# Optimization experiments

Measured on AMD Instinct MI355X. Metric: run time of the kernel, lower is better.

The kernel has to match this reference:

```python
import jax, jax.numpy as jnp
import numpy as np

B, N, K = 8, 4096, 64
D = 256   # d_model
G = 512   # g: number of query points


def _gather(points, idx):
    # points: [B, N, C], idx: [B, G, K] -> [B, G, K, C]
    return jax.vmap(lambda p, i: p[i])(points, idx)


def _mlp(h, W1, b1, W2, b2):
    # torch Linear: y = x @ W.T + b
    return jax.nn.relu(h @ W1.T + b1) @ W2.T + b2


def setup_inputs() -> dict:
    key = jax.random.key(0)
    ks = jax.random.split(key, 12)
    s = 1.0 / np.sqrt(D)
    return {
        "xyz": jax.random.normal(ks[0], (B, N, 3), jnp.float32),
        "x": jax.random.normal(ks[1], (B, N, D), jnp.float32),
        "dist_arg_sort": jax.random.randint(ks[2], (B, N, K), 0, N),
        "Wq": jax.random.normal(ks[3], (D, D), jnp.float32) * s,
        "Wk": jax.random.normal(ks[4], (D, D), jnp.float32) * s,
        "Wv": jax.random.normal(ks[5], (D, D), jnp.float32) * s,
        "Wd1": jax.random.normal(ks[6], (D, 3), jnp.float32) * 0.5,
        "bd1": jnp.zeros((D,), jnp.float32),
        "Wd2": jax.random.normal(ks[7], (D, D), jnp.float32) * s,
        "bd2": jnp.zeros((D,), jnp.float32),
        "Wg1": jax.random.normal(ks[8], (D, D), jnp.float32) * s,
        "bg1": jnp.zeros((D,), jnp.float32),
        "Wg2": jax.random.normal(ks[9], (D, D), jnp.float32) * s,
        "bg2": jnp.zeros((D,), jnp.float32),
    }


def reference(xyz, x, dist_arg_sort, Wq, Wk, Wv, Wd1, bd1, Wd2, bd2, Wg1, bg1, Wg2, bg2):
    g_idx = jnp.sort(dist_arg_sort[:, :G], axis=-1)          # [B,G,K]
    g_xyz = _gather(xyz, g_idx)                               # [B,G,K,3]
    gq = x[:, :G] @ Wq.T                                      # [B,G,D]
    gk = _gather(x @ Wk.T, g_idx)                             # [B,G,K,D]
    gv = _gather(x @ Wv.T, g_idx)                             # [B,G,K,D]
    # positional encoding MLP on coordinate deltas
    g_pos_enc = _mlp(xyz[:, :G, None] - g_xyz, Wd1, bd1, Wd2, bd2)  # [B,G,K,D]
    # vector attention MLP
    g_attn = _mlp(gq[:, :, None] - gk + g_pos_enc, Wg1, bg1, Wg2, bg2)
    g_attn = jax.nn.softmax(g_attn / np.sqrt(D).astype(np.float32), axis=-2)
    # weighted sum over neighbor dim
    return jnp.einsum("bmnf,bmnf->bmf", g_attn, gv + g_pos_enc)  # [B,G,D]
```

## Files before the change

### kernel.cpp

```cpp
#include <hip/hip_runtime.h>

#define DEV static __device__ __forceinline__

typedef __attribute__((ext_vector_type(8))) short bf16x8;
typedef __attribute__((ext_vector_type(4))) float f32x4;
typedef __attribute__((ext_vector_type(4))) unsigned u32x4;

constexpr int BB = 8, NN = 4096, KK = 64, DD = 256, GG = 512;

DEV unsigned short f2b(float f){
  unsigned u = __builtin_bit_cast(unsigned, f);
  unsigned r = (u + 0x7FFFu + ((u >> 16) & 1u)) >> 16;
  return (unsigned short)r;
}
DEV float b2f(unsigned short h){
  unsigned u = ((unsigned)h) << 16;
  return __builtin_bit_cast(float, u);
}
DEV unsigned f2b2(float lo, float hi){
  unsigned r;
  asm("v_cvt_pk_bf16_f32 %0, %1, %2" : "=v"(r) : "v"(lo), "v"(hi));
  return r;
}
DEV int swz(int row, int byteoff){ return row*512 + (byteoff ^ ((row & 15) << 4)); }

DEV f32x4 zero4(){ f32x4 z = {0.f, 0.f, 0.f, 0.f}; return z; }

__global__ void k_detect(const unsigned short* __restrict__ x_raw, int* __restrict__ flag){
  int lane = threadIdx.x;
  float mx = 0.f;
#pragma unroll
  for (int i = 0; i < 16; ++i) mx = fmaxf(mx, fabsf(b2f(x_raw[lane*16 + i])));
  unsigned long long big = __ballot(mx > 1e4f);
  if (lane == 0) *flag = (big == 0ull) ? 1 : 0;
}

struct PrepArgs {
  const void* src[12];
  void*       dst[12];
  int         n[12];
  int         bf16out[12];
};

__global__ void k_prep(PrepArgs P, const int* __restrict__ flagp){
  int flag = *flagp;
  long stride = (long)gridDim.x * blockDim.x;
  long gid = (long)blockIdx.x * blockDim.x + threadIdx.x;
  for (int s = 0; s < 12; ++s){
    int ns = P.n[s];
    const void* sp = P.src[s];
    if (P.bf16out[s]){
      unsigned short* dp = (unsigned short*)P.dst[s];
      for (long i = gid; i < ns; i += stride)
        dp[i] = flag ? ((const unsigned short*)sp)[i] : f2b(((const float*)sp)[i]);
    } else {
      float* dp = (float*)P.dst[s];
      for (long i = gid; i < ns; i += stride)
        dp[i] = flag ? b2f(((const unsigned short*)sp)[i]) : ((const float*)sp)[i];
    }
  }
}

DEV void gemm64(const char* sbuf, const unsigned short* __restrict__ Wt,
                int lane, int c0, f32x4 acc[4][4]){
  const int lrow = lane & 15, lk = lane >> 4;
  const unsigned short* wbase = Wt + (c0 + lrow)*DD + lk*8;
  bf16x8 bcur[4], bnxt[4];
#pragma unroll
  for (int nf = 0; nf < 4; ++nf) bcur[nf] = *(const bf16x8*)(wbase + nf*16*DD);
#pragma unroll
  for (int ks = 0; ks < 8; ++ks){
    bf16x8 a[4];
#pragma unroll
    for (int mf = 0; mf < 4; ++mf)
      a[mf] = *(const bf16x8*)(sbuf + swz(mf*16 + lrow, ks*64 + lk*16));
    if (ks < 7){
#pragma unroll
      for (int nf = 0; nf < 4; ++nf)
        bnxt[nf] = *(const bf16x8*)(wbase + nf*16*DD + (ks + 1)*32);
    }
    __builtin_amdgcn_s_setprio(1);
#pragma unroll
    for (int mf = 0; mf < 4; ++mf)
#pragma unroll
      for (int nf = 0; nf < 4; ++nf)
        acc[mf][nf] = __builtin_amdgcn_mfma_f32_16x16x32_bf16(a[mf], bcur[nf], acc[mf][nf], 0, 0, 0);
    __builtin_amdgcn_s_setprio(0);
#pragma unroll
    for (int nf = 0; nf < 4; ++nf) bcur[nf] = bnxt[nf];
  }
}

DEV void gemm32(const char* sbuf, const unsigned short* __restrict__ Wt,
                int lane, int c0, f32x4 acc[4][2]){
  const int lrow = lane & 15, lk = lane >> 4;
  const unsigned short* wbase = Wt + (c0 + lrow)*DD + lk*8;
  bf16x8 bcur[2], bnxt[2];
#pragma unroll
  for (int nf = 0; nf < 2; ++nf) bcur[nf] = *(const bf16x8*)(wbase + nf*16*DD);
#pragma unroll
  for (int ks = 0; ks < 8; ++ks){
    bf16x8 a[4];
#pragma unroll
    for (int mf = 0; mf < 4; ++mf)
      a[mf] = *(const bf16x8*)(sbuf + swz(mf*16 + lrow, ks*64 + lk*16));
    if (ks < 7){
#pragma unroll
      for (int nf = 0; nf < 2; ++nf)
        bnxt[nf] = *(const bf16x8*)(wbase + nf*16*DD + (ks + 1)*32);
    }
    __builtin_amdgcn_s_setprio(1);
#pragma unroll
    for (int mf = 0; mf < 4; ++mf)
#pragma unroll
      for (int nf = 0; nf < 2; ++nf)
        acc[mf][nf] = __builtin_amdgcn_mfma_f32_16x16x32_bf16(a[mf], bcur[nf], acc[mf][nf], 0, 0, 0);
    __builtin_amdgcn_s_setprio(0);
#pragma unroll
    for (int nf = 0; nf < 2; ++nf) bcur[nf] = bnxt[nf];
  }
}

__global__ __launch_bounds__(256, 2) void k_gemmA(
    const void* __restrict__ x_in,
    const unsigned short* __restrict__ Wq_b, const unsigned short* __restrict__ Wk_b,
    const unsigned short* __restrict__ Wv_b,
    unsigned short* __restrict__ ktab, unsigned short* __restrict__ vtab,
    float* __restrict__ gq, const int* __restrict__ flagp){
  __shared__ __align__(16) char sA[64*512];
  const int tid = threadIdx.x, lane = tid & 63, wv = tid >> 6;
  const int flag = *flagp;
  const long row0 = (long)blockIdx.x * 64;
  const int b = (int)(row0 >> 12), n0 = (int)(row0 & 4095);

#pragma unroll
  for (int it = 0; it < 8; ++it){
    int r = (tid >> 5) + it*8;
    int f0 = (tid & 31)*8;
    bf16x8 v;
    if (flag){
      v = *(const bf16x8*)((const unsigned short*)x_in + (row0 + r)*DD + f0);
    } else {
      const float* xp = (const float*)x_in + (row0 + r)*DD + f0;
      f32x4 lo = *(const f32x4*)xp;
      f32x4 hi = *(const f32x4*)(xp + 4);
      u32x4 t;
#pragma unroll
      for (int e = 0; e < 2; ++e){ t[e] = f2b2(lo[2*e], lo[2*e+1]); t[e+2] = f2b2(hi[2*e], hi[2*e+1]); }
      v = __builtin_bit_cast(bf16x8, t);
    }
    *(bf16x8*)(sA + swz(r, f0*2)) = v;
  }
  __syncthreads();

  const int c0 = wv*64;
  const int nout = (n0 < GG) ? 3 : 2;
  for (int o = 0; o < nout; ++o){
    const unsigned short* Wt = (o == 0) ? Wk_b : (o == 1) ? Wv_b : Wq_b;
    f32x4 acc[4][4];
#pragma unroll
    for (int mf = 0; mf < 4; ++mf)
#pragma unroll
      for (int nf = 0; nf < 4; ++nf) acc[mf][nf] = zero4();
    gemm64(sA, Wt, lane, c0, acc);
#pragma unroll
    for (int mf = 0; mf < 4; ++mf)
#pragma unroll
      for (int nf = 0; nf < 4; ++nf)
#pragma unroll
        for (int r = 0; r < 4; ++r){
          int grow = mf*16 + (lane >> 4)*4 + r;
          int col = c0 + nf*16 + (lane & 15);
          float v = acc[mf][nf][r];
          if (o == 0)      ktab[(row0 + grow)*DD + col] = f2b(v);
          else if (o == 1) vtab[(row0 + grow)*DD + col] = f2b(v);
          else             gq[((long)b*GG + n0 + grow)*DD + col] = v;
        }
  }
}

__global__ __launch_bounds__(512, 4) void k_attn(
    const unsigned short* __restrict__ ktab, const unsigned short* __restrict__ vtab,
    const float* __restrict__ gq, const float* __restrict__ xyzf, const int* __restrict__ didx,
    const unsigned short* __restrict__ Wd2_b, const unsigned short* __restrict__ Wg1_b,
    const unsigned short* __restrict__ Wg2_b,
    const float* __restrict__ Wd1f, const float* __restrict__ bd1f, const float* __restrict__ bd2f,
    const float* __restrict__ bg1f, const float* __restrict__ bg2f,
    void* __restrict__ out, const int* __restrict__ flagp){
  __shared__ __align__(16) char S[64*512];
  __shared__ __align__(16) char U[64*512];
  __shared__ float s_gq[256];
  __shared__ float s_delta[64*3];

  const int tid = threadIdx.x, lane = tid & 63, wv = tid >> 6;
  const int gang = tid >> 5;
  const int f0 = (tid & 31)*8;
  const int flag = *flagp;
  int wg = blockIdx.x;
  wg = (wg & 7)*512 + (wg >> 3);
  const int b = wg >> 9, g = wg & 511;
  const long bN = (long)b * NN;

  int jrow[4];
  {
    const int* dptr = didx + (bN + g)*KK + gang*4;
#pragma unroll
    for (int it = 0; it < 4; ++it) jrow[it] = dptr[it];
  }
  if (tid < 256) s_gq[tid] = gq[((long)b*GG + g)*DD + tid];
  if (tid < 64){
    int j = didx[(bN + g)*KK + tid];
    long qb = (bN + g)*3, jb = (bN + j)*3;
#pragma unroll
    for (int c = 0; c < 3; ++c) s_delta[tid*3 + c] = xyzf[qb + c] - xyzf[jb + c];
  }
  f32x4 w1v[6];
  {
    const f32x4* wp = (const f32x4*)(Wd1f + f0*3);
#pragma unroll
    for (int q = 0; q < 6; ++q) w1v[q] = wp[q];
  }
  f32x4 b1lo = *(const f32x4*)(bd1f + f0), b1hi = *(const f32x4*)(bd1f + f0 + 4);
  const int c0 = wv*32;
  float bg2lo = bg2f[c0 + (lane & 15)];
  float bg2hi = bg2f[c0 + 16 + (lane & 15)];
  __syncthreads();

#pragma unroll
  for (int it = 0; it < 4; ++it){
    int r = gang*4 + it;
    float d0 = s_delta[r*3], d1 = s_delta[r*3+1], d2 = s_delta[r*3+2];
    float h[8];
#pragma unroll
    for (int e = 0; e < 8; ++e){
      float bias = (e < 4) ? b1lo[e] : b1hi[e-4];
      float w0 = w1v[(e*3+0) >> 2][(e*3+0) & 3];
      float w1 = w1v[(e*3+1) >> 2][(e*3+1) & 3];
      float w2 = w1v[(e*3+2) >> 2][(e*3+2) & 3];
      h[e] = fmaxf(fmaf(d0, w0, fmaf(d1, w1, fmaf(d2, w2, bias))), 0.f);
    }
    u32x4 t;
#pragma unroll
    for (int q = 0; q < 4; ++q) t[q] = f2b2(h[2*q], h[2*q+1]);
    *(bf16x8*)(S + swz(r, f0*2)) = __builtin_bit_cast(bf16x8, t);
  }

  bf16x8 kreg[4];
#pragma unroll
  for (int it = 0; it < 4; ++it)
    kreg[it] = *(const bf16x8*)(ktab + (bN + jrow[it])*DD + f0);
  __syncthreads();

  {
    f32x4 acc[4][2];
#pragma unroll
    for (int mf = 0; mf < 4; ++mf)
#pragma unroll
      for (int nf = 0; nf < 2; ++nf) acc[mf][nf] = zero4();
    gemm32(S, Wd2_b, lane, c0, acc);
#pragma unroll
    for (int nf = 0; nf < 2; ++nf){
      float bias = bd2f[c0 + nf*16 + (lane & 15)];
#pragma unroll
      for (int mf = 0; mf < 4; ++mf){
        int row = mf*16 + (lane >> 4)*4;
        int col = c0 + nf*16 + (lane & 15);
#pragma unroll
        for (int h = 0; h < 2; ++h){
          unsigned pk = f2b2(acc[mf][nf][2*h] + bias, acc[mf][nf][2*h+1] + bias);
          *(unsigned short*)(U + swz(row + 2*h,     col*2)) = (unsigned short)(pk & 0xffff);
          *(unsigned short*)(U + swz(row + 2*h + 1, col*2)) = (unsigned short)(pk >> 16);
        }
      }
    }
  }
  __syncthreads();

#pragma unroll
  for (int it = 0; it < 4; ++it){
    int r = gang*4 + it;
    bf16x8 p8 = *(const bf16x8*)(U + swz(r, f0*2));
    float v[8];
#pragma unroll
    for (int e = 0; e < 8; ++e)
      v[e] = s_gq[f0 + e] - b2f((unsigned short)kreg[it][e]) + b2f((unsigned short)p8[e]);
    u32x4 t;
#pragma unroll
    for (int q = 0; q < 4; ++q) t[q] = f2b2(v[2*q], v[2*q+1]);
    *(bf16x8*)(S + swz(r, f0*2)) = __builtin_bit_cast(bf16x8, t);
  }
  __syncthreads();

  {
    f32x4 acc[4][2];
#pragma unroll
    for (int mf = 0; mf < 4; ++mf)
#pragma unroll
      for (int nf = 0; nf < 2; ++nf) acc[mf][nf] = zero4();
    gemm32(S, Wg1_b, lane, c0, acc);
    __syncthreads();
#pragma unroll
    for (int nf = 0; nf < 2; ++nf){
      float bias = bg1f[c0 + nf*16 + (lane & 15)];
#pragma unroll
      for (int mf = 0; mf < 4; ++mf){
        int row = mf*16 + (lane >> 4)*4;
        int col = c0 + nf*16 + (lane & 15);
#pragma unroll
        for (int h = 0; h < 2; ++h){
          unsigned pk = f2b2(fmaxf(acc[mf][nf][2*h] + bias, 0.f),
                             fmaxf(acc[mf][nf][2*h+1] + bias, 0.f));
          *(unsigned short*)(S + swz(row + 2*h,     col*2)) = (unsigned short)(pk & 0xffff);
          *(unsigned short*)(S + swz(row + 2*h + 1, col*2)) = (unsigned short)(pk >> 16);
        }
      }
    }
  }
  __syncthreads();

  f32x4 lg[4][2];
#pragma unroll
  for (int mf = 0; mf < 4; ++mf)
#pragma unroll
    for (int nf = 0; nf < 2; ++nf) lg[mf][nf] = zero4();
  gemm32(S, Wg2_b, lane, c0, lg);
  __syncthreads();

  bf16x8 vreg[4];
#pragma unroll
  for (int it = 0; it < 4; ++it)
    vreg[it] = *(const bf16x8*)(vtab + (bN + jrow[it])*DD + f0);

#pragma unroll
  for (int nf = 0; nf < 2; ++nf){
    float bias = (nf == 0) ? bg2lo : bg2hi;
    float m = -1e30f;
#pragma unroll
    for (int mf = 0; mf < 4; ++mf)
#pragma unroll
      for (int r = 0; r < 4; ++r){ lg[mf][nf][r] += bias; m = fmaxf(m, lg[mf][nf][r]); }
    m = fmaxf(m, __shfl_xor(m, 16));
    m = fmaxf(m, __shfl_xor(m, 32));
    float s = 0.f;
#pragma unroll
    for (int mf = 0; mf < 4; ++mf)
#pragma unroll
      for (int r = 0; r < 4; ++r){
        float e = __expf((lg[mf][nf][r] - m) * 0.0625f);
        lg[mf][nf][r] = e; s += e;
      }
    s += __shfl_xor(s, 16);
    s += __shfl_xor(s, 32);
    float inv = 1.f / s;
#pragma unroll
    for (int mf = 0; mf < 4; ++mf){
      int row = mf*16 + (lane >> 4)*4;
      int col = c0 + nf*16 + (lane & 15);
#pragma unroll
      for (int h = 0; h < 2; ++h){
        unsigned pk = f2b2(lg[mf][nf][2*h] * inv, lg[mf][nf][2*h+1] * inv);
        *(unsigned short*)(S + swz(row + 2*h,     col*2)) = (unsigned short)(pk & 0xffff);
        *(unsigned short*)(S + swz(row + 2*h + 1, col*2)) = (unsigned short)(pk >> 16);
      }
    }
  }
  __syncthreads();

  {
    float accv[8];
#pragma unroll
    for (int e = 0; e < 8; ++e) accv[e] = 0.f;
#pragma unroll
    for (int kk2 = 0; kk2 < 4; ++kk2){
      int row = gang*4 + kk2;
      bf16x8 w8 = *(const bf16x8*)(S + swz(row, f0*2));
      bf16x8 p8 = *(const bf16x8*)(U + swz(row, f0*2));
#pragma unroll
      for (int e = 0; e < 8; ++e)
        accv[e] = fmaf(b2f((unsigned short)w8[e]),
                       b2f((unsigned short)vreg[kk2][e]) + b2f((unsigned short)p8[e]), accv[e]);
    }
    float* red = (float*)(S + gang*2048);
    f32x4 lo = {accv[0], accv[1], accv[2], accv[3]};
    f32x4 hi = {accv[4], accv[5], accv[6], accv[7]};
    *(f32x4*)(red + f0)     = lo;
    *(f32x4*)(red + f0 + 4) = hi;
  }
  __syncthreads();
  if (tid < 256){
    float v = 0.f;
#pragma unroll
    for (int p = 0; p < 16; ++p) v += *(const float*)(S + p*2048 + tid*4);
    long oi = ((long)b*GG + g)*DD + tid;
    if (flag) ((unsigned short*)out)[oi] = f2b(v);
    else      ((float*)out)[oi] = v;
  }
}

extern "C" void kernel_launch(void* const* d_in, const int* in_sizes, int n_in,
                              void* d_out, int out_size, void* d_ws, size_t ws_size,
                              hipStream_t stream){
  char* ws = (char*)d_ws;
  int* flag = (int*)ws;
  unsigned short* ktab = (unsigned short*)(ws + 256);
  unsigned short* vtab = ktab + (size_t)BB*NN*DD;
  float* gq   = (float*)(vtab + (size_t)BB*NN*DD);
  float* xyzf = gq + (size_t)BB*GG*DD;
  unsigned short* Wq_b  = (unsigned short*)(xyzf + (size_t)BB*NN*3);
  unsigned short* Wk_b  = Wq_b  + DD*DD;
  unsigned short* Wv_b  = Wk_b  + DD*DD;
  unsigned short* Wd2_b = Wv_b  + DD*DD;
  unsigned short* Wg1_b = Wd2_b + DD*DD;
  unsigned short* Wg2_b = Wg1_b + DD*DD;
  float* Wd1f = (float*)(Wg2_b + DD*DD);
  float* bd1f = Wd1f + DD*3;
  float* bd2f = bd1f + DD;
  float* bg1f = bd2f + DD;
  float* bg2f = bg1f + DD;

  k_detect<<<1, 64, 0, stream>>>((const unsigned short*)d_in[1], flag);

  PrepArgs P;
  const int wsrc[6] = {3, 4, 5, 8, 10, 12};
  unsigned short* wdst[6] = {Wq_b, Wk_b, Wv_b, Wd2_b, Wg1_b, Wg2_b};
  for (int i = 0; i < 6; ++i){ P.src[i] = d_in[wsrc[i]]; P.dst[i] = wdst[i]; P.n[i] = DD*DD; P.bf16out[i] = 1; }
  P.src[6]  = d_in[0];  P.dst[6]  = xyzf; P.n[6]  = BB*NN*3; P.bf16out[6]  = 0;
  P.src[7]  = d_in[6];  P.dst[7]  = Wd1f; P.n[7]  = DD*3;    P.bf16out[7]  = 0;
  P.src[8]  = d_in[7];  P.dst[8]  = bd1f; P.n[8]  = DD;      P.bf16out[8]  = 0;
  P.src[9]  = d_in[9];  P.dst[9]  = bd2f; P.n[9]  = DD;      P.bf16out[9]  = 0;
  P.src[10] = d_in[11]; P.dst[10] = bg1f; P.n[10] = DD;      P.bf16out[10] = 0;
  P.src[11] = d_in[13]; P.dst[11] = bg2f; P.n[11] = DD;      P.bf16out[11] = 0;
  k_prep<<<256, 256, 0, stream>>>(P, flag);

  k_gemmA<<<512, 256, 0, stream>>>(d_in[1], Wq_b, Wk_b, Wv_b, ktab, vtab, gq, flag);

  k_attn<<<4096, 512, 0, stream>>>(ktab, vtab, gq, xyzf, (const int*)d_in[2],
      Wd2_b, Wg1_b, Wg2_b, Wd1f, bd1f, bd2f, bg1f, bg2f, d_out, flag);
}
```

Before: 282.4 us.

## Replace XOR-swizzled LDS layout with padded row pitch and prefetch first weight fragments

Shared-memory tiles switch from an XOR-swizzled 512-byte row layout to a padded 560-byte pitch, aiming to avoid bank conflicts with simpler address arithmetic. The first B-operand fragments for each small GEMM are also loaded early, before the preceding LDS fill or sync, so global weight latency overlaps other work. The padding raises LDS use per block, which may lower occupancy. Padded strides can also leave different bank-conflict patterns than the swizzle did, for example on the scattered 2-byte stores.

```diff
diff --git a/kernel.cpp b/kernel.cpp
--- a/kernel.cpp
+++ b/kernel.cpp
@@ -7,6 +7,7 @@
 typedef __attribute__((ext_vector_type(4))) unsigned u32x4;
 
 constexpr int BB = 8, NN = 4096, KK = 64, DD = 256, GG = 512;
+constexpr int PITCH = 560;
 
 DEV unsigned short f2b(float f){
   unsigned u = __builtin_bit_cast(unsigned, f);
@@ -22,7 +23,7 @@
   asm("v_cvt_pk_bf16_f32 %0, %1, %2" : "=v"(r) : "v"(lo), "v"(hi));
   return r;
 }
-DEV int swz(int row, int byteoff){ return row*512 + (byteoff ^ ((row & 15) << 4)); }
+DEV int rof(int row, int byteoff){ return row*PITCH + byteoff; }
 
 DEV f32x4 zero4(){ f32x4 z = {0.f, 0.f, 0.f, 0.f}; return z; }
 
@@ -61,6 +62,12 @@
   }
 }
 
+DEV void preB(const unsigned short* __restrict__ Wt, int lane, int c0, bf16x8 b0[2]){
+  const unsigned short* wbase = Wt + (c0 + (lane & 15))*DD + (lane >> 4)*8;
+  b0[0] = *(const bf16x8*)(wbase);
+  b0[1] = *(const bf16x8*)(wbase + 16*DD);
+}
+
 DEV void gemm64(const char* sbuf, const unsigned short* __restrict__ Wt,
                 int lane, int c0, f32x4 acc[4][4]){
   const int lrow = lane & 15, lk = lane >> 4;
@@ -73,7 +80,7 @@
     bf16x8 a[4];
 #pragma unroll
     for (int mf = 0; mf < 4; ++mf)
-      a[mf] = *(const bf16x8*)(sbuf + swz(mf*16 + lrow, ks*64 + lk*16));
+      a[mf] = *(const bf16x8*)(sbuf + rof(mf*16 + lrow, ks*64 + lk*16));
     if (ks < 7){
 #pragma unroll
       for (int nf = 0; nf < 4; ++nf)
@@ -92,18 +99,17 @@
 }
 
 DEV void gemm32(const char* sbuf, const unsigned short* __restrict__ Wt,
-                int lane, int c0, f32x4 acc[4][2]){
+                int lane, int c0, f32x4 acc[4][2], const bf16x8 b0[2]){
   const int lrow = lane & 15, lk = lane >> 4;
   const unsigned short* wbase = Wt + (c0 + lrow)*DD + lk*8;
   bf16x8 bcur[2], bnxt[2];
-#pragma unroll
-  for (int nf = 0; nf < 2; ++nf) bcur[nf] = *(const bf16x8*)(wbase + nf*16*DD);
+  bcur[0] = b0[0]; bcur[1] = b0[1];
 #pragma unroll
   for (int ks = 0; ks < 8; ++ks){
     bf16x8 a[4];
 #pragma unroll
     for (int mf = 0; mf < 4; ++mf)
-      a[mf] = *(const bf16x8*)(sbuf + swz(mf*16 + lrow, ks*64 + lk*16));
+      a[mf] = *(const bf16x8*)(sbuf + rof(mf*16 + lrow, ks*64 + lk*16));
     if (ks < 7){
 #pragma unroll
       for (int nf = 0; nf < 2; ++nf)
@@ -127,7 +133,7 @@
     const unsigned short* __restrict__ Wv_b,
     unsigned short* __restrict__ ktab, unsigned short* __restrict__ vtab,
     float* __restrict__ gq, const int* __restrict__ flagp){
-  __shared__ __align__(16) char sA[64*512];
+  __shared__ __align__(16) char sA[64*PITCH];
   const int tid = threadIdx.x, lane = tid & 63, wv = tid >> 6;
   const int flag = *flagp;
   const long row0 = (long)blockIdx.x * 64;
@@ -149,7 +155,7 @@
       for (int e = 0; e < 2; ++e){ t[e] = f2b2(lo[2*e], lo[2*e+1]); t[e+2] = f2b2(hi[2*e], hi[2*e+1]); }
       v = __builtin_bit_cast(bf16x8, t);
     }
-    *(bf16x8*)(sA + swz(r, f0*2)) = v;
+    *(bf16x8*)(sA + rof(r, f0*2)) = v;
   }
   __syncthreads();
 
@@ -187,8 +193,8 @@
     const float* __restrict__ Wd1f, const float* __restrict__ bd1f, const float* __restrict__ bd2f,
     const float* __restrict__ bg1f, const float* __restrict__ bg2f,
     void* __restrict__ out, const int* __restrict__ flagp){
-  __shared__ __align__(16) char S[64*512];
-  __shared__ __align__(16) char U[64*512];
+  __shared__ __align__(16) char S[64*PITCH];
+  __shared__ __align__(16) char U[64*PITCH];
   __shared__ float s_gq[256];
   __shared__ float s_delta[64*3];
 
@@ -226,6 +232,8 @@
   float bg2hi = bg2f[c0 + 16 + (lane & 15)];
   __syncthreads();
 
+  bf16x8 b0d2[2];
+  preB(Wd2_b, lane, c0, b0d2);
 #pragma unroll
   for (int it = 0; it < 4; ++it){
     int r = gang*4 + it;
@@ -242,7 +250,7 @@
     u32x4 t;
 #pragma unroll
     for (int q = 0; q < 4; ++q) t[q] = f2b2(h[2*q], h[2*q+1]);
-    *(bf16x8*)(S + swz(r, f0*2)) = __builtin_bit_cast(bf16x8, t);
+    *(bf16x8*)(S + rof(r, f0*2)) = __builtin_bit_cast(bf16x8, t);
   }
 
   bf16x8 kreg[4];
@@ -257,7 +265,7 @@
     for (int mf = 0; mf < 4; ++mf)
 #pragma unroll
       for (int nf = 0; nf < 2; ++nf) acc[mf][nf] = zero4();
-    gemm32(S, Wd2_b, lane, c0, acc);
+    gemm32(S, Wd2_b, lane, c0, acc, b0d2);
 #pragma unroll
     for (int nf = 0; nf < 2; ++nf){
       float bias = bd2f[c0 + nf*16 + (lane & 15)];
@@ -268,18 +276,20 @@
 #pragma unroll
         for (int h = 0; h < 2; ++h){
           unsigned pk = f2b2(acc[mf][nf][2*h] + bias, acc[mf][nf][2*h+1] + bias);
-          *(unsigned short*)(U + swz(row + 2*h,     col*2)) = (unsigned short)(pk & 0xffff);
-          *(unsigned short*)(U + swz(row + 2*h + 1, col*2)) = (unsigned short)(pk >> 16);
+          *(unsigned short*)(U + rof(row + 2*h,     col*2)) = (unsigned short)(pk & 0xffff);
+          *(unsigned short*)(U + rof(row + 2*h + 1, col*2)) = (unsigned short)(pk >> 16);
         }
       }
     }
   }
   __syncthreads();
 
+  bf16x8 b0g1[2];
+  preB(Wg1_b, lane, c0, b0g1);
 #pragma unroll
   for (int it = 0; it < 4; ++it){
     int r = gang*4 + it;
-    bf16x8 p8 = *(const bf16x8*)(U + swz(r, f0*2));
+    bf16x8 p8 = *(const bf16x8*)(U + rof(r, f0*2));
     float v[8];
 #pragma unroll
     for (int e = 0; e < 8; ++e)
@@ -287,17 +297,19 @@
     u32x4 t;
 #pragma unroll
     for (int q = 0; q < 4; ++q) t[q] = f2b2(v[2*q], v[2*q+1]);
-    *(bf16x8*)(S + swz(r, f0*2)) = __builtin_bit_cast(bf16x8, t);
-  }
-  __syncthreads();
-
+    *(bf16x8*)(S + rof(r, f0*2)) = __builtin_bit_cast(bf16x8, t);
+  }
+  __syncthreads();
+
+  bf16x8 b0g2[2];
   {
     f32x4 acc[4][2];
 #pragma unroll
     for (int mf = 0; mf < 4; ++mf)
 #pragma unroll
       for (int nf = 0; nf < 2; ++nf) acc[mf][nf] = zero4();
-    gemm32(S, Wg1_b, lane, c0, acc);
+    gemm32(S, Wg1_b, lane, c0, acc, b0g1);
+    preB(Wg2_b, lane, c0, b0g2);
     __syncthreads();
 #pragma unroll
     for (int nf = 0; nf < 2; ++nf){
@@ -310,8 +322,8 @@
         for (int h = 0; h < 2; ++h){
           unsigned pk = f2b2(fmaxf(acc[mf][nf][2*h] + bias, 0.f),
                              fmaxf(acc[mf][nf][2*h+1] + bias, 0.f));
-          *(unsigned short*)(S + swz(row + 2*h,     col*2)) = (unsigned short)(pk & 0xffff);
-          *(unsigned short*)(S + swz(row + 2*h + 1, col*2)) = (unsigned short)(pk >> 16);
+          *(unsigned short*)(S + rof(row + 2*h,     col*2)) = (unsigned short)(pk & 0xffff);
+          *(unsigned short*)(S + rof(row + 2*h + 1, col*2)) = (unsigned short)(pk >> 16);
         }
       }
     }
@@ -323,7 +335,7 @@
   for (int mf = 0; mf < 4; ++mf)
 #pragma unroll
     for (int nf = 0; nf < 2; ++nf) lg[mf][nf] = zero4();
-  gemm32(S, Wg2_b, lane, c0, lg);
+  gemm32(S, Wg2_b, lane, c0, lg, b0g2);
   __syncthreads();
 
   bf16x8 vreg[4];
@@ -359,8 +371,8 @@
 #pragma unroll
       for (int h = 0; h < 2; ++h){
         unsigned pk = f2b2(lg[mf][nf][2*h] * inv, lg[mf][nf][2*h+1] * inv);
-        *(unsigned short*)(S + swz(row + 2*h,     col*2)) = (unsigned short)(pk & 0xffff);
-        *(unsigned short*)(S + swz(row + 2*h + 1, col*2)) = (unsigned short)(pk >> 16);
+        *(unsigned short*)(S + rof(row + 2*h,     col*2)) = (unsigned short)(pk & 0xffff);
+        *(unsigned short*)(S + rof(row + 2*h + 1, col*2)) = (unsigned short)(pk >> 16);
       }
     }
   }
@@ -373,14 +385,14 @@
 #pragma unroll
     for (int kk2 = 0; kk2 < 4; ++kk2){
       int row = gang*4 + kk2;
-      bf16x8 w8 = *(const bf16x8*)(S + swz(row, f0*2));
-      bf16x8 p8 = *(const bf16x8*)(U + swz(row, f0*2));
+      bf16x8 w8 = *(const bf16x8*)(S + rof(row, f0*2));
+      bf16x8 p8 = *(const bf16x8*)(U + rof(row, f0*2));
 #pragma unroll
       for (int e = 0; e < 8; ++e)
         accv[e] = fmaf(b2f((unsigned short)w8[e]),
                        b2f((unsigned short)vreg[kk2][e]) + b2f((unsigned short)p8[e]), accv[e]);
     }
-    float* red = (float*)(S + gang*2048);
+    float* red = (float*)(S + gang*4*PITCH);
     f32x4 lo = {accv[0], accv[1], accv[2], accv[3]};
     f32x4 hi = {accv[4], accv[5], accv[6], accv[7]};
     *(f32x4*)(red + f0)     = lo;
@@ -390,7 +402,7 @@
   if (tid < 256){
     float v = 0.f;
 #pragma unroll
-    for (int p = 0; p < 16; ++p) v += *(const float*)(S + p*2048 + tid*4);
+    for (int p = 0; p < 16; ++p) v += *(const float*)(S + p*4*PITCH + tid*4);
     long oi = ((long)b*GG + g)*DD + tid;
     if (flag) ((unsigned short*)out)[oi] = f2b(v);
     else      ((float*)out)[oi] = v;
```

New measurement: 270.0 us, median of 2. 4.4% less time.
